# Optimization experiments

Hardware: AMD Instinct MI355X
Metric: run time of the kernel (lower is better)

Reference implementation:

```python
import jax, jax.numpy as jnp
import numpy as np

# Large finite negative used for masking inside the softmax chain. exp(NEG - m)
# underflows to exactly 0.0 in fp32, so valid positions match the torch -inf
# masking bit-for-bit; masked output positions are set to -inf at the end.
NEG = jnp.float32(-1e30)

B, L, F = 8192, 128, 64


def setup_inputs() -> dict:
    key = jax.random.key(0)
    k1, k2, k3 = jax.random.split(key, 3)
    return {
        "choice_set_features": jax.random.normal(k1, (B, L, F), dtype=jnp.float32),
        "choice_set_lengths": jax.random.randint(k2, (B,), 1, L + 1),  # in [1, L]
        "thetas": jax.random.uniform(k3, (F, F), dtype=jnp.float32),   # torch.rand init
        "mixture_weights": jnp.ones((F,), dtype=jnp.float32),
    }


def reference(choice_set_features, choice_set_lengths, thetas, mixture_weights):
    b, l, f = choice_set_features.shape
    # utilities[b,l,g] = x[b,l,:] @ thetas[g,:]   (x @ thetas.T)
    util = jnp.einsum('blf,gf->blg', choice_set_features, thetas)
    pad = jnp.arange(l)[None, :] >= choice_set_lengths[:, None]  # [B, L] True = padded
    util = jnp.where(pad[..., None], NEG, util)
    # log_softmax over the choice-set dimension (dim 1), per mixture component
    log_probs = jax.nn.log_softmax(util, axis=1)
    # mixture over components (dim 2) with log-softmaxed mixture weights
    out = jax.nn.logsumexp(log_probs + jax.nn.log_softmax(mixture_weights), axis=2)
    # padded slots are exactly -inf in the torch reference
    return jnp.where(pad, -jnp.inf, out)
```

## Files before the change

### kernel.cpp

```cpp
#include <hip/hip_runtime.h>
#include <math.h>

#define NEGV  (-1e30f)
#define LOG2E 1.44269504088896340736f
#define LN2   0.69314718055994530942f

typedef __attribute__((ext_vector_type(8))) _Float16 half8;
typedef __attribute__((ext_vector_type(2))) __fp16   fp16x2;
typedef __attribute__((ext_vector_type(4))) float f32x4;

__device__ __forceinline__ float exp2_fast(float a) { return __builtin_amdgcn_exp2f(a); }
__device__ __forceinline__ float log2_fast(float a) { return __builtin_amdgcn_logf(a); }

__device__ __forceinline__ half8 cvt8(float4 a, float4 b) {
    union { half8 v; fp16x2 p[4]; } u;
    u.p[0] = __builtin_amdgcn_cvt_pkrtz(a.x, a.y);
    u.p[1] = __builtin_amdgcn_cvt_pkrtz(a.z, a.w);
    u.p[2] = __builtin_amdgcn_cvt_pkrtz(b.x, b.y);
    u.p[3] = __builtin_amdgcn_cvt_pkrtz(b.z, b.w);
    return u.v;
}

__global__ __launch_bounds__(256, 6) void mixed_logit_kernel(
    const float* __restrict__ x,
    const int*   __restrict__ lens,
    const float* __restrict__ theta,
    const float* __restrict__ mw,
    float* __restrict__ out)
{
    __shared__ __align__(16) unsigned char xbuf[128 * 144];
    __shared__ float red_s[4][128];

    const int tid  = threadIdx.x;
    const int lane = tid & 63;
    const int w    = tid >> 6;
    const int c15  = lane & 15;
    const int q    = lane >> 4;
    const int b    = blockIdx.x;
    const int len  = lens[b];

    float4 ra[8];
    {
        const float4* xp = (const float4*)(x + (size_t)b * 8192);
#pragma unroll
        for (int i = 0; i < 4; ++i) {
            const int j2 = (i << 8) + tid;
            ra[2 * i]     = xp[j2 * 2];
            ra[2 * i + 1] = xp[j2 * 2 + 1];
        }
    }

    half8 th[2];
    float wg[4];
    {
        const float* tr = theta + (size_t)((w << 4) + c15) * 64 + (q << 3);
#pragma unroll
        for (int kt = 0; kt < 2; ++kt) {
            float4 a = *(const float4*)(tr + kt * 32);
            float4 c = *(const float4*)(tr + kt * 32 + 4);
            a.x *= LOG2E; a.y *= LOG2E; a.z *= LOG2E; a.w *= LOG2E;
            c.x *= LOG2E; c.y *= LOG2E; c.z *= LOG2E; c.w *= LOG2E;
            th[kt] = cvt8(a, c);
        }
        const float mwl = mw[lane];
        float mmax = mwl;
#pragma unroll
        for (int s = 32; s >= 1; s >>= 1) mmax = fmaxf(mmax, __shfl_xor(mmax, s, 64));
        float me = __expf(mwl - mmax);
#pragma unroll
        for (int s = 32; s >= 1; s >>= 1) me += __shfl_xor(me, s, 64);
        const float logZ = mmax + __logf(me);
#pragma unroll
        for (int i = 0; i < 4; ++i)
            wg[i] = (mw[(w << 4) + (q << 2) + i] - logZ) * LOG2E;
    }

#pragma unroll
    for (int i = 0; i < 4; ++i) {
        const int j2 = (i << 8) + tid;
        const half8 h = cvt8(ra[2 * i], ra[2 * i + 1]);
        *(half8*)(xbuf + (j2 >> 3) * 144 + (j2 & 7) * 16) = h;
    }
    __syncthreads();

    f32x4 acc[8];
#pragma unroll
    for (int nt = 0; nt < 8; ++nt) acc[nt] = (f32x4){0.f, 0.f, 0.f, 0.f};

#pragma unroll
    for (int nt = 0; nt < 8; ++nt) {
        const unsigned char* rb = xbuf + ((nt << 4) + c15) * 144 + (q << 4);
        const half8 x0 = *(const half8*)(rb);
        const half8 x1 = *(const half8*)(rb + 64);
        acc[nt] = __builtin_amdgcn_mfma_f32_16x16x32_f16(th[0], x0, acc[nt], 0, 0, 0);
        acc[nt] = __builtin_amdgcn_mfma_f32_16x16x32_f16(th[1], x1, acc[nt], 0, 0, 0);
    }

#pragma unroll
    for (int nt = 0; nt < 8; ++nt) {
        const bool v = ((nt << 4) + c15) < len;
#pragma unroll
        for (int i = 0; i < 4; ++i) {
            const float pv = exp2_fast(acc[nt][i]);
            acc[nt][i] = v ? pv : 0.f;
        }
    }

    float e4[4];
#pragma unroll
    for (int i = 0; i < 4; ++i) {
        float e = 0.f;
#pragma unroll
        for (int nt = 0; nt < 8; ++nt) e += acc[nt][i];
#pragma unroll
        for (int s = 1; s < 16; s <<= 1) e += __shfl_xor(e, s, 64);
        e4[i] = exp2_fast(wg[i] - log2_fast(e));
    }

#pragma unroll
    for (int nt = 0; nt < 8; ++nt) {
        float s2 = acc[nt][0] * e4[0];
        s2 = fmaf(acc[nt][1], e4[1], s2);
        s2 = fmaf(acc[nt][2], e4[2], s2);
        s2 = fmaf(acc[nt][3], e4[3], s2);
        s2 += __shfl_xor(s2, 16, 64);
        s2 += __shfl_xor(s2, 32, 64);
        if ((nt >> 1) == q) {
            red_s[w][(nt << 4) + c15] = s2;
        }
    }
    __syncthreads();

    if (tid < 128) {
        const int l = tid;
        const float S = red_s[0][l] + red_s[1][l] + red_s[2][l] + red_s[3][l];
        const float o = LN2 * log2_fast(S);
        out[(size_t)b * 128 + l] = (l < len) ? o : NEGV;
    }
}

extern "C" void kernel_launch(void* const* d_in, const int* in_sizes, int n_in,
                              void* d_out, int out_size, void* d_ws, size_t ws_size,
                              hipStream_t stream) {
    const float* x     = (const float*)d_in[0];
    const int*   lens  = (const int*)d_in[1];
    const float* theta = (const float*)d_in[2];
    const float* mw    = (const float*)d_in[3];
    float* out = (float*)d_out;
    const int B = in_sizes[1];
    mixed_logit_kernel<<<B, 256, 0, stream>>>(x, lens, theta, mw, out);
}
```

Before: 44.41 us.

## Halve block size so each wave computes two theta tiles

Result: no change. 44.92 us (+1.2%).

```diff
diff --git a/kernel.cpp b/kernel.cpp
--- a/kernel.cpp
+++ b/kernel.cpp
@@ -21,7 +21,7 @@
     return u.v;
 }
 
-__global__ __launch_bounds__(256, 6) void mixed_logit_kernel(
+__global__ __launch_bounds__(128, 4) void mixed_logit_kernel(
     const float* __restrict__ x,
     const int*   __restrict__ lens,
     const float* __restrict__ theta,
@@ -29,7 +29,7 @@
     float* __restrict__ out)
 {
     __shared__ __align__(16) unsigned char xbuf[128 * 144];
-    __shared__ float red_s[4][128];
+    __shared__ float red_s[2][128];
 
     const int tid  = threadIdx.x;
     const int lane = tid & 63;
@@ -39,28 +39,32 @@
     const int b    = blockIdx.x;
     const int len  = lens[b];
 
-    float4 ra[8];
+    float4 ra[16];
     {
         const float4* xp = (const float4*)(x + (size_t)b * 8192);
 #pragma unroll
-        for (int i = 0; i < 4; ++i) {
-            const int j2 = (i << 8) + tid;
+        for (int i = 0; i < 8; ++i) {
+            const int j2 = (i << 7) + tid;
             ra[2 * i]     = xp[j2 * 2];
             ra[2 * i + 1] = xp[j2 * 2 + 1];
         }
     }
 
-    half8 th[2];
-    float wg[4];
+    half8 th[2][2];
+    float wg[2][4];
     {
-        const float* tr = theta + (size_t)((w << 4) + c15) * 64 + (q << 3);
 #pragma unroll
-        for (int kt = 0; kt < 2; ++kt) {
-            float4 a = *(const float4*)(tr + kt * 32);
-            float4 c = *(const float4*)(tr + kt * 32 + 4);
-            a.x *= LOG2E; a.y *= LOG2E; a.z *= LOG2E; a.w *= LOG2E;
-            c.x *= LOG2E; c.y *= LOG2E; c.z *= LOG2E; c.w *= LOG2E;
-            th[kt] = cvt8(a, c);
+        for (int j = 0; j < 2; ++j) {
+            const int gt = (w << 1) + j;
+            const float* tr = theta + (size_t)((gt << 4) + c15) * 64 + (q << 3);
+#pragma unroll
+            for (int kt = 0; kt < 2; ++kt) {
+                float4 a = *(const float4*)(tr + kt * 32);
+                float4 c = *(const float4*)(tr + kt * 32 + 4);
+                a.x *= LOG2E; a.y *= LOG2E; a.z *= LOG2E; a.w *= LOG2E;
+                c.x *= LOG2E; c.y *= LOG2E; c.z *= LOG2E; c.w *= LOG2E;
+                th[j][kt] = cvt8(a, c);
+            }
         }
         const float mwl = mw[lane];
         float mmax = mwl;
@@ -71,58 +75,77 @@
         for (int s = 32; s >= 1; s >>= 1) me += __shfl_xor(me, s, 64);
         const float logZ = mmax + __logf(me);
 #pragma unroll
-        for (int i = 0; i < 4; ++i)
-            wg[i] = (mw[(w << 4) + (q << 2) + i] - logZ) * LOG2E;
+        for (int j = 0; j < 2; ++j) {
+            const int gt = (w << 1) + j;
+#pragma unroll
+            for (int i = 0; i < 4; ++i)
+                wg[j][i] = (mw[(gt << 4) + (q << 2) + i] - logZ) * LOG2E;
+        }
     }
 
 #pragma unroll
-    for (int i = 0; i < 4; ++i) {
-        const int j2 = (i << 8) + tid;
+    for (int i = 0; i < 8; ++i) {
+        const int j2 = (i << 7) + tid;
         const half8 h = cvt8(ra[2 * i], ra[2 * i + 1]);
         *(half8*)(xbuf + (j2 >> 3) * 144 + (j2 & 7) * 16) = h;
     }
     __syncthreads();
 
-    f32x4 acc[8];
+    f32x4 acc[2][8];
 #pragma unroll
-    for (int nt = 0; nt < 8; ++nt) acc[nt] = (f32x4){0.f, 0.f, 0.f, 0.f};
+    for (int j = 0; j < 2; ++j)
+#pragma unroll
+        for (int nt = 0; nt < 8; ++nt) acc[j][nt] = (f32x4){0.f, 0.f, 0.f, 0.f};
 
 #pragma unroll
     for (int nt = 0; nt < 8; ++nt) {
         const unsigned char* rb = xbuf + ((nt << 4) + c15) * 144 + (q << 4);
         const half8 x0 = *(const half8*)(rb);
         const half8 x1 = *(const half8*)(rb + 64);
-        acc[nt] = __builtin_amdgcn_mfma_f32_16x16x32_f16(th[0], x0, acc[nt], 0, 0, 0);
-        acc[nt] = __builtin_amdgcn_mfma_f32_16x16x32_f16(th[1], x1, acc[nt], 0, 0, 0);
+#pragma unroll
+        for (int j = 0; j < 2; ++j) {
+            acc[j][nt] = __builtin_amdgcn_mfma_f32_16x16x32_f16(th[j][0], x0, acc[j][nt], 0, 0, 0);
+            acc[j][nt] = __builtin_amdgcn_mfma_f32_16x16x32_f16(th[j][1], x1, acc[j][nt], 0, 0, 0);
+        }
     }
+
+    bool vm[8];
+#pragma unroll
+    for (int nt = 0; nt < 8; ++nt) vm[nt] = ((nt << 4) + c15) < len;
+
+#pragma unroll
+    for (int j = 0; j < 2; ++j)
+#pragma unroll
+        for (int nt = 0; nt < 8; ++nt)
+#pragma unroll
+            for (int i = 0; i < 4; ++i) {
+                const float pv = exp2_fast(acc[j][nt][i]);
+                acc[j][nt][i] = vm[nt] ? pv : 0.f;
+            }
+
+    float e4[2][4];
+#pragma unroll
+    for (int j = 0; j < 2; ++j)
+#pragma unroll
+        for (int i = 0; i < 4; ++i) {
+            float e = 0.f;
+#pragma unroll
+            for (int nt = 0; nt < 8; ++nt) e += acc[j][nt][i];
+#pragma unroll
+            for (int s = 1; s < 16; s <<= 1) e += __shfl_xor(e, s, 64);
+            e4[j][i] = exp2_fast(wg[j][i] - log2_fast(e));
+        }
 
 #pragma unroll
     for (int nt = 0; nt < 8; ++nt) {
-        const bool v = ((nt << 4) + c15) < len;
-#pragma unroll
-        for (int i = 0; i < 4; ++i) {
-            const float pv = exp2_fast(acc[nt][i]);
-            acc[nt][i] = v ? pv : 0.f;
-        }
-    }
-
-    float e4[4];
-#pragma unroll
-    for (int i = 0; i < 4; ++i) {
-        float e = 0.f;
-#pragma unroll
-        for (int nt = 0; nt < 8; ++nt) e += acc[nt][i];
-#pragma unroll
-        for (int s = 1; s < 16; s <<= 1) e += __shfl_xor(e, s, 64);
-        e4[i] = exp2_fast(wg[i] - log2_fast(e));
-    }
-
-#pragma unroll
-    for (int nt = 0; nt < 8; ++nt) {
-        float s2 = acc[nt][0] * e4[0];
-        s2 = fmaf(acc[nt][1], e4[1], s2);
-        s2 = fmaf(acc[nt][2], e4[2], s2);
-        s2 = fmaf(acc[nt][3], e4[3], s2);
+        float s2 = acc[0][nt][0] * e4[0][0];
+        s2 = fmaf(acc[0][nt][1], e4[0][1], s2);
+        s2 = fmaf(acc[0][nt][2], e4[0][2], s2);
+        s2 = fmaf(acc[0][nt][3], e4[0][3], s2);
+        s2 = fmaf(acc[1][nt][0], e4[1][0], s2);
+        s2 = fmaf(acc[1][nt][1], e4[1][1], s2);
+        s2 = fmaf(acc[1][nt][2], e4[1][2], s2);
+        s2 = fmaf(acc[1][nt][3], e4[1][3], s2);
         s2 += __shfl_xor(s2, 16, 64);
         s2 += __shfl_xor(s2, 32, 64);
         if ((nt >> 1) == q) {
@@ -131,9 +154,9 @@
     }
     __syncthreads();
 
-    if (tid < 128) {
+    {
         const int l = tid;
-        const float S = red_s[0][l] + red_s[1][l] + red_s[2][l] + red_s[3][l];
+        const float S = red_s[0][l] + red_s[1][l];
         const float o = LN2 * log2_fast(S);
         out[(size_t)b * 128 + l] = (l < len) ? o : NEGV;
     }
@@ -148,5 +171,5 @@
     const float* mw    = (const float*)d_in[3];
     float* out = (float*)d_out;
     const int B = in_sizes[1];
-    mixed_logit_kernel<<<B, 256, 0, stream>>>(x, lens, theta, mw, out);
+    mixed_logit_kernel<<<B, 128, 0, stream>>>(x, lens, theta, mw, out);
 }
```
